# Performance work log

Measured on AMD Instinct MI355X. Metric: run time of the kernel, lower is better.

Reference implementation:

```python
import jax, jax.numpy as jnp
import numpy as np

S, D = 8192, 2048      # sequence length, feature dim (input_size)
H, E, K, L = 64, 64, 2, 64  # gate hidden, expert count, top-k, expert layer_size
EPS = 1e-12            # torch F.normalize eps


def setup_inputs() -> dict:
    key = jax.random.key(0)
    ks = jax.random.split(key, 5)
    x = jax.random.normal(ks[0], (S, D), dtype=jnp.float32)
    # torch nn.Linear weights have shape [out_features, in_features]
    Wg_in = jax.random.normal(ks[1], (H, D), dtype=jnp.float32) * 0.02   # gate.input
    Wg_lin = jax.random.normal(ks[2], (E, H), dtype=jnp.float32) * 0.02  # gate.linear
    Wg_out = jax.random.normal(ks[3], (1, S), dtype=jnp.float32) * 0.02  # gate.output
    We = jax.random.normal(ks[4], (E, L, D), dtype=jnp.float32) * 0.02   # expert weight bank
    return {"x": x, "Wg_in": Wg_in, "Wg_lin": Wg_lin, "Wg_out": Wg_out, "We": We}


def reference(x, Wg_in, Wg_lin, Wg_out, We):
    # --- SparseGate (eval mode: dropout = identity) ---
    h = x @ Wg_in.T                         # [S, H]
    logits = h @ Wg_lin.T                   # [S, E]
    scores = (logits.T @ Wg_out.T)[:, 0]    # Linear(S,1) applied to [E,S] -> [E]
    topv, idx = jax.lax.top_k(scores, K)    # global top-k experts for whole input
    g = jax.nn.softmax(topv)                # softmax over the k selected logits

    # --- dispatch to k selected experts (FFNN: Linear -> normalize(-1) -> GELU) ---
    Wsel = We[idx]                          # [K, L, D]
    z = jnp.einsum('sd,kld->ksl', x, Wsel)  # [K, S, L]
    z = z / jnp.maximum(jnp.linalg.norm(z, axis=-1, keepdims=True), EPS)
    z = jax.nn.gelu(z, approximate=False)   # torch GELU default is exact erf

    # --- weighted combine: sum_k g_k * expert_k(x) ---
    return jnp.einsum('k,ksl->sl', g, z)    # [S, L]
```

## Files before the change

### kernel.cpp

```cpp
#include <hip/hip_runtime.h>
#include <hip/hip_bf16.h>
#include <math.h>

#define D_DIM 2048
#define L_DIM 64
#define E_NUM 64
#define H_DIM 64

typedef float f32x4_t __attribute__((ext_vector_type(4)));
typedef __bf16 bf16x8_t __attribute__((ext_vector_type(8)));

#define WS_UPART 0u
#define WS_U     (512u * 2048u * 4u)
#define WS_V     (WS_U + 2048u * 4u)
#define WS_META  (WS_V + 256u)
#define WS_WB    (WS_META + 64u)
#define WS_XB    (WS_WB + 128u * 2048u * 2u)
#define WS_PART  (WS_XB + 8192u * 2048u * 2u)


__global__ void k_upart(const float* __restrict__ x, const float* __restrict__ wout,
                        float* __restrict__ upart, __hip_bfloat16* __restrict__ xbt) {
  const int t = threadIdx.x;
  const int d8 = t * 8;
  const int s0 = blockIdx.x * 16;
  const int kstep = d8 >> 6;
  const int kc = (d8 >> 3) & 7;
  float a0 = 0.f, a1 = 0.f, a2 = 0.f, a3 = 0.f;
  float a4 = 0.f, a5 = 0.f, a6 = 0.f, a7 = 0.f;
  for (int i = 0; i < 16; ++i) {
    const int row = s0 + i;
    const float w = wout[row];
    const float4 pa = *reinterpret_cast<const float4*>(x + (size_t)row * D_DIM + d8);
    const float4 pb = *reinterpret_cast<const float4*>(x + (size_t)row * D_DIM + d8 + 4);
    a0 += pa.x * w; a1 += pa.y * w; a2 += pa.z * w; a3 += pa.w * w;
    a4 += pb.x * w; a5 += pb.y * w; a6 += pb.z * w; a7 += pb.w * w;
    union { __hip_bfloat16 h[8]; uint4 u; } pk;
    pk.h[0] = __float2bfloat16(pa.x); pk.h[1] = __float2bfloat16(pa.y);
    pk.h[2] = __float2bfloat16(pa.z); pk.h[3] = __float2bfloat16(pa.w);
    pk.h[4] = __float2bfloat16(pb.x); pk.h[5] = __float2bfloat16(pb.y);
    pk.h[6] = __float2bfloat16(pb.z); pk.h[7] = __float2bfloat16(pb.w);
    const int mt = row >> 7, rl = row & 127;
    const size_t off = (size_t)mt * 262144 + kstep * 8192 + rl * 64 +
                       ((kc ^ (rl & 7)) * 8);
    *reinterpret_cast<uint4*>(xbt + off) = pk.u;
  }
  float* up = upart + (size_t)blockIdx.x * D_DIM + d8;
  *reinterpret_cast<float4*>(up)     = make_float4(a0, a1, a2, a3);
  *reinterpret_cast<float4*>(up + 4) = make_float4(a4, a5, a6, a7);
}

__global__ void k_ufinish(const float* __restrict__ upart, float* __restrict__ u) {
  const int d = blockIdx.x * 256 + threadIdx.x;
  float s = 0.f;
#pragma unroll 8
  for (int c = 0; c < 512; ++c) s += upart[(size_t)c * D_DIM + d];
  u[d] = s;
}

__global__ void k_v(const float* __restrict__ wg_in, const float* __restrict__ u,
                    float* __restrict__ v) {
  const int h = blockIdx.x;
  const int t = threadIdx.x;
  const float4* wr = reinterpret_cast<const float4*>(wg_in + (size_t)h * D_DIM);
  const float4* ur = reinterpret_cast<const float4*>(u);
  float s = 0.f;
#pragma unroll
  for (int i = t; i < 512; i += 256) {
    const float4 a = wr[i];
    const float4 b = ur[i];
    s += a.x * b.x + a.y * b.y + a.z * b.z + a.w * b.w;
  }
  __shared__ float red[4];
#pragma unroll
  for (int off = 32; off; off >>= 1) s += __shfl_down(s, off, 64);
  if ((t & 63) == 0) red[t >> 6] = s;
  __syncthreads();
  if (t == 0) v[h] = red[0] + red[1] + red[2] + red[3];
}

__global__ void k_gate(const float* __restrict__ wg_lin, const float* __restrict__ v,
                       int* __restrict__ sel, float* __restrict__ g) {
  __shared__ float vv[H_DIM];
  __shared__ float sc[E_NUM];
  const int t = threadIdx.x;
  vv[t] = v[t];
  __syncthreads();
  float s = 0.f;
#pragma unroll 8
  for (int hh = 0; hh < H_DIM; ++hh) s += wg_lin[t * H_DIM + hh] * vv[hh];
  sc[t] = s;
  __syncthreads();
  if (t == 0) {
    int b1 = 0; float m1 = sc[0];
    for (int e = 1; e < E_NUM; ++e) { if (sc[e] > m1) { m1 = sc[e]; b1 = e; } }
    int b2 = -1; float m2 = -3.4e38f;
    for (int e = 0; e < E_NUM; ++e) {
      if (e != b1 && sc[e] > m2) { m2 = sc[e]; b2 = e; }
    }
    const float e2 = expf(m2 - m1);
    const float g0 = 1.0f / (1.0f + e2);
    sel[0] = b1; sel[1] = b2;
    g[0] = g0; g[1] = 1.0f - g0;
  }
}

__global__ void k_wb(const float* __restrict__ we, const int* __restrict__ sel,
                     __hip_bfloat16* __restrict__ wbt) {
  const int n = blockIdx.x;
  const int e = sel[n >> 6];
  const int l = n & 63;
  const float* src = we + ((size_t)e * L_DIM + l) * D_DIM;
  const int t = threadIdx.x;
  const int d8 = t * 8;
  const int kstep = d8 >> 6;
  const int kc = (d8 >> 3) & 7;
  const float4 a = reinterpret_cast<const float4*>(src)[2 * t];
  const float4 b = reinterpret_cast<const float4*>(src)[2 * t + 1];
  union { __hip_bfloat16 h[8]; uint4 u; } pk;
  pk.h[0] = __float2bfloat16(a.x); pk.h[1] = __float2bfloat16(a.y);
  pk.h[2] = __float2bfloat16(a.z); pk.h[3] = __float2bfloat16(a.w);
  pk.h[4] = __float2bfloat16(b.x); pk.h[5] = __float2bfloat16(b.y);
  pk.h[6] = __float2bfloat16(b.z); pk.h[7] = __float2bfloat16(b.w);
  const size_t off = (size_t)kstep * 8192 + n * 64 + ((kc ^ (n & 7)) * 8);
  *reinterpret_cast<uint4*>(wbt + off) = pk.u;
}

__device__ __forceinline__ void async_ld16(const void* gp, void* lp) {
  __builtin_amdgcn_global_load_lds(
      (const __attribute__((address_space(1))) unsigned int*)gp,
      (__attribute__((address_space(3))) unsigned int*)lp, 16, 0, 0);
}

__device__ __forceinline__ float gelu_f(float v) {
  return 0.5f * v * (1.0f + erff(v * 0.70710678118654752440f));
}

__global__ __launch_bounds__(512) void k_moe_gemm(
    const __hip_bfloat16* __restrict__ xbt, const __hip_bfloat16* __restrict__ wbt,
    float* __restrict__ part) {
  __shared__ __align__(16) unsigned char lds[2][32768];

  const int tid = threadIdx.x;
  const int w = tid >> 6, lane = tid & 63;
  const int wm = w >> 2, wn = w & 3;
  const int m0 = blockIdx.x * 128;
  const int kg = blockIdx.y;
  const int fr = lane & 15, fq = lane >> 4;
  const size_t abase = (size_t)blockIdx.x * 262144;

  f32x4_t acc[4][2];
#pragma unroll
  for (int mf = 0; mf < 4; ++mf)
#pragma unroll
    for (int nf = 0; nf < 2; ++nf) acc[mf][nf] = (f32x4_t){0.f, 0.f, 0.f, 0.f};

  auto stage = [&](int buf, int kk) {
    const size_t tbase = (size_t)(kg * 8 + kk) * 8192;
#pragma unroll
    for (int ph = 0; ph < 2; ++ph) {
      const int c = ph * 512 + tid;
      async_ld16(xbt + abase + tbase + c * 8, &lds[buf][c * 16]);
      async_ld16(wbt + tbase + c * 8, &lds[buf][16384 + c * 16]);
    }
  };

  stage(0, 0);
  __syncthreads();
  for (int kk = 0; kk < 8; ++kk) {
    const int cur = kk & 1;
    if (kk < 7) stage(cur ^ 1, kk + 1);
    const unsigned char* ldsA = lds[cur];
    const unsigned char* ldsB = lds[cur] + 16384;
    union fragu { uint4 u; bf16x8_t v; };
    fragu af[4][2], bf_[2][2];
#pragma unroll
    for (int mf = 0; mf < 4; ++mf)
#pragma unroll
      for (int ks = 0; ks < 2; ++ks) {
        const int ar = wm * 64 + mf * 16 + fr;
        const int kq = ks * 4 + fq;
        af[mf][ks].u = *reinterpret_cast<const uint4*>(
            ldsA + ar * 128 + ((kq ^ (ar & 7)) * 16));
      }
#pragma unroll
    for (int nf = 0; nf < 2; ++nf)
#pragma unroll
      for (int ks = 0; ks < 2; ++ks) {
        const int br = wn * 32 + nf * 16 + fr;
        const int kq = ks * 4 + fq;
        bf_[nf][ks].u = *reinterpret_cast<const uint4*>(
            ldsB + br * 128 + ((kq ^ (br & 7)) * 16));
      }
#pragma unroll
    for (int mf = 0; mf < 4; ++mf)
#pragma unroll
      for (int nf = 0; nf < 2; ++nf) {
        acc[mf][nf] = __builtin_amdgcn_mfma_f32_16x16x32_bf16(
            af[mf][0].v, bf_[nf][0].v, acc[mf][nf], 0, 0, 0);
        acc[mf][nf] = __builtin_amdgcn_mfma_f32_16x16x32_bf16(
            af[mf][1].v, bf_[nf][1].v, acc[mf][nf], 0, 0, 0);
      }
    __syncthreads();
  }

  float* z = reinterpret_cast<float*>(lds);
#pragma unroll
  for (int mf = 0; mf < 4; ++mf)
#pragma unroll
    for (int nf = 0; nf < 2; ++nf)
#pragma unroll
      for (int reg = 0; reg < 4; ++reg)
        z[(wm * 64 + mf * 16 + fq * 4 + reg) * 128 + wn * 32 + nf * 16 + fr] =
            acc[mf][nf][reg];
  __syncthreads();
#pragma unroll
  for (int p = 0; p < 8; ++p) {
    const int idx = p * 512 + tid;
    const int r = idx >> 5, c4 = (idx & 31) * 4;
    *reinterpret_cast<f32x4_t*>(part + ((size_t)kg * 8192 + m0 + r) * 128 + c4) =
        *reinterpret_cast<const f32x4_t*>(z + r * 128 + c4);
  }
}

__global__ __launch_bounds__(256) void k_finish(const float* __restrict__ part,
                                                const float* __restrict__ gw,
                                                float* __restrict__ out) {
  __shared__ float z[32 * 132];
  __shared__ float ps[32 * 8];
  const int tid = threadIdx.x;
  const int m0 = blockIdx.x * 32;
  const float g0 = gw[0], g1 = gw[1];
  const size_t KSTRIDE = (size_t)8192 * 128;
#pragma unroll
  for (int p = 0; p < 4; ++p) {
    const int idx = p * 256 + tid;
    const int r = idx >> 5, c4 = (idx & 31) * 4;
    const float* pp = part + ((size_t)(m0 + r)) * 128 + c4;
    const f32x4_t s = *reinterpret_cast<const f32x4_t*>(pp)
                    + *reinterpret_cast<const f32x4_t*>(pp + KSTRIDE)
                    + *reinterpret_cast<const f32x4_t*>(pp + 2 * KSTRIDE)
                    + *reinterpret_cast<const f32x4_t*>(pp + 3 * KSTRIDE);
    z[r * 132 + c4 + 0] = s[0];
    z[r * 132 + c4 + 1] = s[1];
    z[r * 132 + c4 + 2] = s[2];
    z[r * 132 + c4 + 3] = s[3];
  }
  __syncthreads();
  {
    const int r = tid >> 3, seg = tid & 7;
    float s = 0.f;
#pragma unroll
    for (int i2 = 0; i2 < 16; ++i2) {
      const float t2 = z[r * 132 + seg * 16 + i2];
      s += t2 * t2;
    }
    ps[r * 8 + seg] = s;
  }
  __syncthreads();
  {
    const int r = tid >> 3, j = tid & 7;
    const float s0 = ps[r * 8 + 0] + ps[r * 8 + 1] + ps[r * 8 + 2] + ps[r * 8 + 3];
    const float s1 = ps[r * 8 + 4] + ps[r * 8 + 5] + ps[r * 8 + 6] + ps[r * 8 + 7];
    const float i0 = 1.0f / fmaxf(sqrtf(s0), 1e-12f);
    const float i1 = 1.0f / fmaxf(sqrtf(s1), 1e-12f);
    float o[8];
#pragma unroll
    for (int i2 = 0; i2 < 8; ++i2) {
      const int c = j * 8 + i2;
      const float za = z[r * 132 + c] * i0;
      const float zb2 = z[r * 132 + 64 + c] * i1;
      o[i2] = g0 * gelu_f(za) + g1 * gelu_f(zb2);
    }
    float4* op = reinterpret_cast<float4*>(out + (size_t)(m0 + r) * 64 + j * 8);
    op[0] = make_float4(o[0], o[1], o[2], o[3]);
    op[1] = make_float4(o[4], o[5], o[6], o[7]);
  }
}

extern "C" void kernel_launch(void* const* d_in, const int* in_sizes, int n_in,
                              void* d_out, int out_size, void* d_ws, size_t ws_size,
                              hipStream_t stream) {
  (void)in_sizes; (void)n_in; (void)out_size; (void)ws_size;
  const float* x      = (const float*)d_in[0];
  const float* wg_in  = (const float*)d_in[1];
  const float* wg_lin = (const float*)d_in[2];
  const float* wg_out = (const float*)d_in[3];
  const float* we     = (const float*)d_in[4];
  float* out = (float*)d_out;
  char* ws = (char*)d_ws;

  float* upart = (float*)(ws + WS_UPART);
  float* u     = (float*)(ws + WS_U);
  float* v     = (float*)(ws + WS_V);
  int*   sel   = (int*)(ws + WS_META);
  float* g     = (float*)(ws + WS_META + 8);
  __hip_bfloat16* wbt = (__hip_bfloat16*)(ws + WS_WB);
  __hip_bfloat16* xbt = (__hip_bfloat16*)(ws + WS_XB);
  float* part = (float*)(ws + WS_PART);

  k_upart  <<<512, 256, 0, stream>>>(x, wg_out, upart, xbt);
  k_ufinish<<<8, 256, 0, stream>>>(upart, u);
  k_v      <<<64, 256, 0, stream>>>(wg_in, u, v);
  k_gate   <<<1, 64, 0, stream>>>(wg_lin, v, sel, g);
  k_wb     <<<128, 256, 0, stream>>>(we, sel, wbt);
  k_moe_gemm<<<dim3(64, 4), 512, 0, stream>>>(xbt, wbt, part);
  k_finish <<<256, 256, 0, stream>>>(part, g, out);
}
```

Before: 184.2 us.

## Retile MoE GEMM into smaller blocks with deeper split-K

The expert GEMM moves from 256 blocks of 512 threads (128-row tiles, 8 double-buffered k-steps) to 1024 blocks of 256 threads (64-row tiles, 4 single-buffered k-steps), with split-K raised from 4 to 8. The LDS epilogue is dropped: accumulators are stored straight to the partial buffer, and the finish kernel now sums 8 partials. The aim is more blocks and higher occupancy to hide latency. In exchange, partial-sum traffic doubles, load/compute overlap from double buffering is lost, and stores are narrower.

```diff
diff --git a/kernel.cpp b/kernel.cpp
--- a/kernel.cpp
+++ b/kernel.cpp
@@ -136,91 +136,84 @@
   return 0.5f * v * (1.0f + erff(v * 0.70710678118654752440f));
 }
 
-__global__ __launch_bounds__(512) void k_moe_gemm(
+__global__ __launch_bounds__(256, 4) void k_moe_gemm(
     const __hip_bfloat16* __restrict__ xbt, const __hip_bfloat16* __restrict__ wbt,
     float* __restrict__ part) {
-  __shared__ __align__(16) unsigned char lds[2][32768];
+  __shared__ __align__(16) unsigned char lds[24576];
 
   const int tid = threadIdx.x;
   const int w = tid >> 6, lane = tid & 63;
-  const int wm = w >> 2, wn = w & 3;
-  const int m0 = blockIdx.x * 128;
+  const int wm = w >> 1, wn = w & 1;
+  const int mb = blockIdx.x;
   const int kg = blockIdx.y;
   const int fr = lane & 15, fq = lane >> 4;
-  const size_t abase = (size_t)blockIdx.x * 262144;
-
-  f32x4_t acc[4][2];
-#pragma unroll
-  for (int mf = 0; mf < 4; ++mf)
-#pragma unroll
-    for (int nf = 0; nf < 2; ++nf) acc[mf][nf] = (f32x4_t){0.f, 0.f, 0.f, 0.f};
-
-  auto stage = [&](int buf, int kk) {
-    const size_t tbase = (size_t)(kg * 8 + kk) * 8192;
+
+  unsigned char* ldsA = lds;
+  unsigned char* ldsB = lds + 8192;
+
+  const size_t abase = (size_t)(mb >> 1) * 262144 + (size_t)(mb & 1) * 4096;
+
+  f32x4_t acc[2][4];
+#pragma unroll
+  for (int mf = 0; mf < 2; ++mf)
+#pragma unroll
+    for (int nf = 0; nf < 4; ++nf) acc[mf][nf] = (f32x4_t){0.f, 0.f, 0.f, 0.f};
+
+  for (int kk = 0; kk < 4; ++kk) {
+    const size_t tbase = (size_t)(kg * 4 + kk) * 8192;
+    if (kk) __syncthreads();
 #pragma unroll
     for (int ph = 0; ph < 2; ++ph) {
-      const int c = ph * 512 + tid;
-      async_ld16(xbt + abase + tbase + c * 8, &lds[buf][c * 16]);
-      async_ld16(wbt + tbase + c * 8, &lds[buf][16384 + c * 16]);
-    }
-  };
-
-  stage(0, 0);
-  __syncthreads();
-  for (int kk = 0; kk < 8; ++kk) {
-    const int cur = kk & 1;
-    if (kk < 7) stage(cur ^ 1, kk + 1);
-    const unsigned char* ldsA = lds[cur];
-    const unsigned char* ldsB = lds[cur] + 16384;
+      const int c = ph * 256 + tid;
+      async_ld16(xbt + abase + tbase + c * 8, ldsA + c * 16);
+    }
+#pragma unroll
+    for (int ph = 0; ph < 4; ++ph) {
+      const int c = ph * 256 + tid;
+      async_ld16(wbt + tbase + c * 8, ldsB + c * 16);
+    }
+    __syncthreads();
     union fragu { uint4 u; bf16x8_t v; };
-    fragu af[4][2], bf_[2][2];
-#pragma unroll
-    for (int mf = 0; mf < 4; ++mf)
+    fragu af[2][2], bf_[4][2];
+#pragma unroll
+    for (int mf = 0; mf < 2; ++mf)
 #pragma unroll
       for (int ks = 0; ks < 2; ++ks) {
-        const int ar = wm * 64 + mf * 16 + fr;
+        const int ar = wm * 32 + mf * 16 + fr;
         const int kq = ks * 4 + fq;
         af[mf][ks].u = *reinterpret_cast<const uint4*>(
             ldsA + ar * 128 + ((kq ^ (ar & 7)) * 16));
       }
 #pragma unroll
-    for (int nf = 0; nf < 2; ++nf)
+    for (int nf = 0; nf < 4; ++nf)
 #pragma unroll
       for (int ks = 0; ks < 2; ++ks) {
-        const int br = wn * 32 + nf * 16 + fr;
+        const int br = wn * 64 + nf * 16 + fr;
         const int kq = ks * 4 + fq;
         bf_[nf][ks].u = *reinterpret_cast<const uint4*>(
             ldsB + br * 128 + ((kq ^ (br & 7)) * 16));
       }
 #pragma unroll
-    for (int mf = 0; mf < 4; ++mf)
-#pragma unroll
-      for (int nf = 0; nf < 2; ++nf) {
+    for (int mf = 0; mf < 2; ++mf)
+#pragma unroll
+      for (int nf = 0; nf < 4; ++nf) {
         acc[mf][nf] = __builtin_amdgcn_mfma_f32_16x16x32_bf16(
             af[mf][0].v, bf_[nf][0].v, acc[mf][nf], 0, 0, 0);
         acc[mf][nf] = __builtin_amdgcn_mfma_f32_16x16x32_bf16(
             af[mf][1].v, bf_[nf][1].v, acc[mf][nf], 0, 0, 0);
       }
-    __syncthreads();
-  }
-
-  float* z = reinterpret_cast<float*>(lds);
-#pragma unroll
-  for (int mf = 0; mf < 4; ++mf)
-#pragma unroll
-    for (int nf = 0; nf < 2; ++nf)
-#pragma unroll
-      for (int reg = 0; reg < 4; ++reg)
-        z[(wm * 64 + mf * 16 + fq * 4 + reg) * 128 + wn * 32 + nf * 16 + fr] =
-            acc[mf][nf][reg];
-  __syncthreads();
-#pragma unroll
-  for (int p = 0; p < 8; ++p) {
-    const int idx = p * 512 + tid;
-    const int r = idx >> 5, c4 = (idx & 31) * 4;
-    *reinterpret_cast<f32x4_t*>(part + ((size_t)kg * 8192 + m0 + r) * 128 + c4) =
-        *reinterpret_cast<const f32x4_t*>(z + r * 128 + c4);
-  }
+  }
+
+#pragma unroll
+  for (int mf = 0; mf < 2; ++mf)
+#pragma unroll
+    for (int nf = 0; nf < 4; ++nf)
+#pragma unroll
+      for (int reg = 0; reg < 4; ++reg) {
+        const int r = mb * 64 + wm * 32 + mf * 16 + fq * 4 + reg;
+        const int c = wn * 64 + nf * 16 + fr;
+        part[((size_t)kg * 8192 + r) * 128 + c] = acc[mf][nf][reg];
+      }
 }
 
 __global__ __launch_bounds__(256) void k_finish(const float* __restrict__ part,
@@ -237,10 +230,10 @@
     const int idx = p * 256 + tid;
     const int r = idx >> 5, c4 = (idx & 31) * 4;
     const float* pp = part + ((size_t)(m0 + r)) * 128 + c4;
-    const f32x4_t s = *reinterpret_cast<const f32x4_t*>(pp)
-                    + *reinterpret_cast<const f32x4_t*>(pp + KSTRIDE)
-                    + *reinterpret_cast<const f32x4_t*>(pp + 2 * KSTRIDE)
-                    + *reinterpret_cast<const f32x4_t*>(pp + 3 * KSTRIDE);
+    f32x4_t s = (f32x4_t){0.f, 0.f, 0.f, 0.f};
+#pragma unroll
+    for (int kgi = 0; kgi < 8; ++kgi)
+      s = s + *reinterpret_cast<const f32x4_t*>(pp + kgi * KSTRIDE);
     z[r * 132 + c4 + 0] = s[0];
     z[r * 132 + c4 + 1] = s[1];
     z[r * 132 + c4 + 2] = s[2];
@@ -304,6 +297,6 @@
   k_v      <<<64, 256, 0, stream>>>(wg_in, u, v);
   k_gate   <<<1, 64, 0, stream>>>(wg_lin, v, sel, g);
   k_wb     <<<128, 256, 0, stream>>>(we, sel, wbt);
-  k_moe_gemm<<<dim3(64, 4), 512, 0, stream>>>(xbt, wbt, part);
+  k_moe_gemm<<<dim3(128, 8), 256, 0, stream>>>(xbt, wbt, part);
   k_finish <<<256, 256, 0, stream>>>(part, g, out);
 }
```

Measured after the change: 185.0 us. About the same (+0.4%).
